# Performance work log

Hardware: AMD Instinct MI355X
Metric: run time of the kernel (lower is better)

## Reference

```python
import jax, jax.numpy as jnp
import numpy as np

N = 200000          # nodes
E = 6400000         # edges (before self-loops)
L = 4               # layer_n
H = 9               # hidden_channels (hardcoded in module)
G = 2000            # graphs in batch
C = 2               # num_classes
NEG_SLOPE = 0.2     # GATConv default leaky_relu slope for attention logits


def setup_inputs() -> dict:
    key = jax.random.key(0)
    ks = jax.random.split(key, 9)
    x = jax.random.normal(ks[0], (N, H), dtype=jnp.float32)
    edge_index = jax.random.randint(ks[1], (2, E), 0, N, dtype=jnp.int32)
    batch = jnp.sort(jax.random.randint(ks[2], (N,), 0, G, dtype=jnp.int32))
    W = jax.random.normal(ks[3], (L, H, H), dtype=jnp.float32) * 0.3
    att_src = jax.random.normal(ks[4], (L, H), dtype=jnp.float32) * 0.3
    att_dst = jax.random.normal(ks[5], (L, H), dtype=jnp.float32) * 0.3
    bias = jax.random.normal(ks[6], (L, H), dtype=jnp.float32) * 0.1
    fc_w = jax.random.normal(ks[7], (L * H, C), dtype=jnp.float32) * 0.2
    fc_b = jax.random.normal(ks[8], (C,), dtype=jnp.float32) * 0.1
    return dict(x=x, edge_index=edge_index, batch=batch, W=W,
                att_src=att_src, att_dst=att_dst, bias=bias,
                fc_w=fc_w, fc_b=fc_b)


def _gat_layer(x, W_l, a_src, a_dst, b_l, src, dst, n):
    # h: [N, H] transformed features (linear, no bias per PyG default)
    h = x @ W_l
    alpha_s = h @ a_src            # [N]
    alpha_d = h @ a_dst            # [N]
    # attention logits per edge (src -> dst), GAT softmax grouped by dst
    e = jax.nn.leaky_relu(alpha_s[src] + alpha_d[dst], NEG_SLOPE)  # [E']
    e = e - jax.ops.segment_max(e, dst, num_segments=n)[dst]
    w = jnp.exp(e)
    denom = jax.ops.segment_sum(w, dst, num_segments=n)[dst]
    alpha = w / denom              # [E']
    out = jax.ops.segment_sum(alpha[:, None] * h[src], dst, num_segments=n)
    return out + b_l


def reference(x, edge_index, batch, W, att_src, att_dst, bias, fc_w, fc_b):
    n = x.shape[0]
    loops = jnp.arange(n, dtype=edge_index.dtype)
    src = jnp.concatenate([edge_index[0], loops])  # add_self_loops=True
    dst = jnp.concatenate([edge_index[1], loops])
    jk = []
    h = x
    for l in range(L):
        h = _gat_layer(h, W[l], att_src[l], att_dst[l], bias[l], src, dst, n)
        h = jax.nn.relu(h)
        jk.append(h)
    jk = jnp.concatenate(jk, axis=1)               # [N, L*H]
    pooled = jax.ops.segment_max(jk, batch, num_segments=G)
    pooled = jnp.where(jnp.isfinite(pooled), pooled, 0.0)  # guard empty graphs
    # dropout is identity at inference
    return pooled @ fc_w + fc_b
```

## Files before the change

### kernel.cpp

```cpp
#include <hip/hip_runtime.h>
#include <hip/hip_fp16.h>

#define Nn 200000
#define Ee 6400000
#define EP 6600000
#define Hh 9
#define Ll 4
#define Gg 2000
#define Cc 2
#define JK 36
#define NCB ((Nn + 1023) >> 10)
#define EPB 8192
#define NBLKA ((EP + EPB - 1) / EPB)
#define NB ((Nn + 255) / 256)
#define NPB 32
#define NAB (Nn / NPB)
#define CAP 3072
#define CAPB 36864
#define HTS (NCB + 1)

union H2F { __half2 h; float f; };


__global__ __launch_bounds__(256) void kA_scatter(
    const int* __restrict__ src, const int* __restrict__ dst,
    int* __restrict__ ctot, int* __restrict__ histT,
    unsigned* __restrict__ bucketed)
{
    __shared__ unsigned pbuf[EPB];
    __shared__ int lh[NCB];
    __shared__ int s[256];
    int t = threadIdx.x;
    if (t < NCB) lh[t] = 0;
    __syncthreads();
    const int base = blockIdx.x * EPB;
    const int nseg = min(EPB, EP - base);
    for (int j = t; j < nseg; j += 256) {
        int e = base + j;
        int d = (e < Ee) ? dst[e] : (e - Ee);
        atomicAdd(&lh[d >> 10], 1);
    }
    __syncthreads();
    int v = (t < NCB) ? lh[t] : 0;
    s[t] = v; __syncthreads();
    for (int off = 1; off < 256; off <<= 1) {
        int u = (t >= off) ? s[t - off] : 0;
        __syncthreads();
        s[t] += u;
        __syncthreads();
    }
    int* hrow = histT + (size_t)blockIdx.x * HTS;
    if (t < NCB) {
        int ex = s[t] - v;
        lh[t] = ex;
        hrow[t] = ex;
        if (v) atomicAdd(&ctot[t], v);
    }
    if (t == 0) hrow[NCB] = nseg;
    __syncthreads();
    for (int j = t; j < nseg; j += 256) {
        int e = base + j;
        int sv, d;
        if (e < Ee) { sv = src[e]; d = dst[e]; } else { sv = e - Ee; d = sv; }
        int pos = atomicAdd(&lh[d >> 10], 1);
        pbuf[pos] = (unsigned)sv | ((unsigned)(d & 1023) << 18);
    }
    __syncthreads();
    for (int j = t; j < nseg; j += 256)
        bucketed[base + j] = pbuf[j];
}

__global__ __launch_bounds__(256) void k_scan(
    const int* __restrict__ ctot, int* __restrict__ cbase,
    int* __restrict__ row_ptr)
{
    __shared__ int s[256];
    int t = threadIdx.x;
    int v = (t < NCB) ? ctot[t] : 0;
    s[t] = v; __syncthreads();
    for (int off = 1; off < 256; off <<= 1) {
        int u = (t >= off) ? s[t - off] : 0;
        __syncthreads();
        s[t] += u;
        __syncthreads();
    }
    if (t < NCB) cbase[t] = s[t] - v;
    if (t == 0) { cbase[NCB] = EP; row_ptr[Nn] = EP; }
}

__global__ __launch_bounds__(1024) void kB_csr(
    const unsigned* __restrict__ bucketed, const int* __restrict__ histT,
    const int* __restrict__ cbase, int* __restrict__ row_ptr,
    int* __restrict__ csr_src)
{
    __shared__ int2 hb[NBLKA];
    __shared__ int bh[1024];
    __shared__ unsigned pbuf[CAPB];
    const int k = blockIdx.x;
    const int t = threadIdx.x;
    const int w = t >> 6, lane = t & 63;
    bh[t] = 0;
    for (int j = t; j < NBLKA; j += 1024) {
        const int* hrow = histT + (size_t)j * HTS + k;
        hb[j] = make_int2(hrow[0], hrow[1]);
    }
    __syncthreads();
    for (int b = w; b < NBLKA; b += 16 * 4) {
        int2 es[4]; unsigned ps[4];
#pragma unroll
        for (int u = 0; u < 4; ++u) {
            int bb = b + 16 * u;
            int2 e = (bb < NBLKA) ? hb[bb] : make_int2(0, 0);
            es[u] = e;
            int j = e.x + lane;
            ps[u] = (j < e.y)
                ? __builtin_nontemporal_load(bucketed + (size_t)bb * EPB + j)
                : 0u;
        }
#pragma unroll
        for (int u = 0; u < 4; ++u) {
            int bb = b + 16 * u;
            if (bb >= NBLKA) break;
            int j = es[u].x + lane;
            if (j < es[u].y) atomicAdd(&bh[(ps[u] >> 18) & 1023], 1);
            for (j += 64; j < es[u].y; j += 64) {
                unsigned p = __builtin_nontemporal_load(
                    bucketed + (size_t)bb * EPB + j);
                atomicAdd(&bh[(p >> 18) & 1023], 1);
            }
        }
    }
    __syncthreads();
    int v = bh[t];
    for (int off = 1; off < 1024; off <<= 1) {
        int u = (t >= off) ? bh[t - off] : 0;
        __syncthreads();
        bh[t] += u;
        __syncthreads();
    }
    const int base_k = cbase[k];
    const int nseg_b = cbase[k + 1] - base_k;
    int ex = bh[t] - v;
    const int node = (k << 10) + t;
    if (node < Nn) row_ptr[node] = base_k + ex;
    bh[t] = ex;
    __syncthreads();
    const bool fit = (nseg_b <= CAPB);
    if (fit) {
        for (int b = w; b < NBLKA; b += 16 * 4) {
            int2 es[4]; unsigned ps[4];
#pragma unroll
            for (int u = 0; u < 4; ++u) {
                int bb = b + 16 * u;
                int2 e = (bb < NBLKA) ? hb[bb] : make_int2(0, 0);
                es[u] = e;
                int j = e.x + lane;
                ps[u] = (j < e.y)
                    ? __builtin_nontemporal_load(bucketed + (size_t)bb * EPB + j)
                    : 0u;
            }
#pragma unroll
            for (int u = 0; u < 4; ++u) {
                int bb = b + 16 * u;
                if (bb >= NBLKA) break;
                int j = es[u].x + lane;
                if (j < es[u].y) {
                    unsigned p = ps[u];
                    int pos = atomicAdd(&bh[(p >> 18) & 1023], 1);
                    pbuf[pos] = p & 0x3FFFFu;
                }
                for (j += 64; j < es[u].y; j += 64) {
                    unsigned p = __builtin_nontemporal_load(
                        bucketed + (size_t)bb * EPB + j);
                    int pos = atomicAdd(&bh[(p >> 18) & 1023], 1);
                    pbuf[pos] = p & 0x3FFFFu;
                }
            }
        }
        __syncthreads();
        for (int j = t; j < nseg_b; j += 1024)
            csr_src[base_k + j] = (int)pbuf[j];
    } else {
        for (int b = w; b < NBLKA; b += 16) {
            int2 e = hb[b];
            int rb = b * EPB;
            for (int j = e.x + lane; j < e.y; j += 64) {
                unsigned p = bucketed[rb + j];
                int pos = base_k + atomicAdd(&bh[(p >> 18) & 1023], 1);
                csr_src[pos] = (int)(p & 0x3FFFFu);
            }
        }
    }
}


__global__ __launch_bounds__(256) void k_transform(
    const float* __restrict__ xin, int xstride,
    const float* __restrict__ Wl,
    const float* __restrict__ adst,
    float4* __restrict__ A, __half* __restrict__ Bh, float* __restrict__ D)
{
    int i = blockIdx.x * blockDim.x + threadIdx.x;
    if (i >= Nn) return;
    const float* xp = xin + (size_t)i * xstride;
    float xi[Hh];
#pragma unroll
    for (int k = 0; k < Hh; ++k) xi[k] = xp[k];
    float hv[Hh];
#pragma unroll
    for (int j = 0; j < Hh; ++j) {
        float s = 0.f;
#pragma unroll
        for (int k = 0; k < Hh; ++k) s += xi[k] * Wl[k * Hh + j];
        hv[j] = s;
    }
    float ad = 0.f;
#pragma unroll
    for (int j = 0; j < Hh; ++j) ad += hv[j] * adst[j];
    H2F u01, u23, u45, u67;
    u01.h = __floats2half2_rn(hv[0], hv[1]);
    u23.h = __floats2half2_rn(hv[2], hv[3]);
    u45.h = __floats2half2_rn(hv[4], hv[5]);
    u67.h = __floats2half2_rn(hv[6], hv[7]);
    A[i] = make_float4(u01.f, u23.f, u45.f, u67.f);
    Bh[i] = __float2half(hv[8]);
    D[i] = ad;
}

__global__ __launch_bounds__(256) void k_node_agg(
    const int* __restrict__ rp, const int* __restrict__ csr,
    const float4* __restrict__ A, const __half* __restrict__ Bh,
    const float* __restrict__ D, const float* __restrict__ asrc,
    const float* __restrict__ biasl,
    float* __restrict__ jk, int l)
{
    __shared__ int scsr[CAP];
    __shared__ int srp[NPB + 1];
    const int nbase = blockIdx.x * NPB;
    const int t = threadIdx.x;
    if (t <= NPB) srp[t] = rp[nbase + t];
    __syncthreads();
    const int beg_blk = srp[0];
    const int nseg = srp[NPB] - beg_blk;
    const bool use_lds = (nseg <= CAP);
    if (use_lds)
        for (int j = t; j < nseg; j += 256)
            scsr[j] = __builtin_nontemporal_load(csr + beg_blk + j);
    __syncthreads();

    const float s0 = asrc[0], s1 = asrc[1], s2 = asrc[2], s3 = asrc[3],
                s4 = asrc[4], s5 = asrc[5], s6 = asrc[6], s7 = asrc[7],
                s8 = asrc[8];

    const int ni = t >> 3;
    const int q  = t & 7;
    const int i  = nbase + ni;
    const float c = D[i];
    float a0=0,a1=0,a2=0,a3=0,a4=0,a5=0,a6=0,a7=0,a8=0,den=0;
    if (use_lds) {
        int idx = srp[ni] - beg_blk + q;
        const int iend = srp[ni + 1] - beg_blk;
        int s = (idx < iend) ? scsr[idx] : 0;
        float4 F = A[s];
        __half hb = Bh[s];
        while (idx < iend) {
            int nidx = idx + 8;
            int sn = (nidx < iend) ? scsr[nidx] : 0;
            float4 Fn = A[sn];
            __half hbn = Bh[sn];
            H2F u; float2 p;
            u.f = F.x; p = __half22float2(u.h); float x0 = p.x, x1 = p.y;
            u.f = F.y; p = __half22float2(u.h); float x2 = p.x, x3 = p.y;
            u.f = F.z; p = __half22float2(u.h); float x4 = p.x, x5 = p.y;
            u.f = F.w; p = __half22float2(u.h); float x6 = p.x, x7 = p.y;
            float x8 = __half2float(hb);
            float as = x0*s0 + x1*s1 + x2*s2 + x3*s3 + x4*s4
                     + x5*s5 + x6*s6 + x7*s7 + x8*s8;
            float lg = as + c;
            lg = lg > 0.f ? lg : 0.2f * lg;
            float w = __expf(lg);
            a0 += w*x0; a1 += w*x1; a2 += w*x2; a3 += w*x3; a4 += w*x4;
            a5 += w*x5; a6 += w*x6; a7 += w*x7; a8 += w*x8;
            den += w;
            F = Fn; hb = hbn; idx = nidx;
        }
    } else {
        for (int e = srp[ni] + q; e < srp[ni + 1]; e += 8) {
            int s = csr[e];
            float4 F = A[s];
            __half hb = Bh[s];
            H2F u; float2 p;
            u.f = F.x; p = __half22float2(u.h); float x0 = p.x, x1 = p.y;
            u.f = F.y; p = __half22float2(u.h); float x2 = p.x, x3 = p.y;
            u.f = F.z; p = __half22float2(u.h); float x4 = p.x, x5 = p.y;
            u.f = F.w; p = __half22float2(u.h); float x6 = p.x, x7 = p.y;
            float x8 = __half2float(hb);
            float as = x0*s0 + x1*s1 + x2*s2 + x3*s3 + x4*s4
                     + x5*s5 + x6*s6 + x7*s7 + x8*s8;
            float lg = as + c;
            lg = lg > 0.f ? lg : 0.2f * lg;
            float w = __expf(lg);
            a0 += w*x0; a1 += w*x1; a2 += w*x2; a3 += w*x3; a4 += w*x4;
            a5 += w*x5; a6 += w*x6; a7 += w*x7; a8 += w*x8;
            den += w;
        }
    }
#pragma unroll
    for (int m = 1; m <= 4; m <<= 1) {
        a0 += __shfl_xor(a0, m); a1 += __shfl_xor(a1, m);
        a2 += __shfl_xor(a2, m); a3 += __shfl_xor(a3, m);
        a4 += __shfl_xor(a4, m); a5 += __shfl_xor(a5, m);
        a6 += __shfl_xor(a6, m); a7 += __shfl_xor(a7, m);
        a8 += __shfl_xor(a8, m); den += __shfl_xor(den, m);
    }
    if (q == 0) {
        float inv = 1.f / den;
        float* jp = jk + (size_t)i * JK + l * Hh;
        float o;
        o = fmaxf(a0*inv + biasl[0], 0.f); __builtin_nontemporal_store(o, jp + 0);
        o = fmaxf(a1*inv + biasl[1], 0.f); __builtin_nontemporal_store(o, jp + 1);
        o = fmaxf(a2*inv + biasl[2], 0.f); __builtin_nontemporal_store(o, jp + 2);
        o = fmaxf(a3*inv + biasl[3], 0.f); __builtin_nontemporal_store(o, jp + 3);
        o = fmaxf(a4*inv + biasl[4], 0.f); __builtin_nontemporal_store(o, jp + 4);
        o = fmaxf(a5*inv + biasl[5], 0.f); __builtin_nontemporal_store(o, jp + 5);
        o = fmaxf(a6*inv + biasl[6], 0.f); __builtin_nontemporal_store(o, jp + 6);
        o = fmaxf(a7*inv + biasl[7], 0.f); __builtin_nontemporal_store(o, jp + 7);
        o = fmaxf(a8*inv + biasl[8], 0.f); __builtin_nontemporal_store(o, jp + 8);
    }
}


__global__ __launch_bounds__(256) void k_graph_ptr(
    const int* __restrict__ batch, int* __restrict__ gp)
{
    int i = blockIdx.x * 256 + threadIdx.x;
    if (i >= Nn) return;
    int b = batch[i];
    if (i == 0) {
        for (int g = 0; g <= b; ++g) gp[g] = 0;
    } else {
        int pb = batch[i - 1];
        for (int g = pb + 1; g <= b; ++g) gp[g] = i;
    }
    if (i == Nn - 1) {
        for (int g = b + 1; g <= Gg; ++g) gp[g] = Nn;
    }
}

__global__ __launch_bounds__(256) void k_pool_seg(
    const float* __restrict__ jk, const int* __restrict__ gp,
    float* __restrict__ pooled)
{
    int t = blockIdx.x * 256 + threadIdx.x;
    if (t >= Gg * JK) return;
    int g = t / JK, col = t - g * JK;
    int beg = gp[g], end = gp[g + 1];
    float m = 0.f;
    for (int i = beg; i < end; ++i)
        m = fmaxf(m, jk[(size_t)i * JK + col]);
    pooled[t] = m;
}

__global__ __launch_bounds__(256) void k_fc(
    const float* __restrict__ pooled, const float* __restrict__ fcw,
    const float* __restrict__ fcb, float* __restrict__ out)
{
    int t = blockIdx.x * blockDim.x + threadIdx.x;
    if (t >= Gg * Cc) return;
    int g = t / Cc, c = t - g * Cc;
    float s = fcb[c];
    const float* pp = pooled + (size_t)g * JK;
#pragma unroll
    for (int j = 0; j < JK; ++j) s += pp[j] * fcw[j * Cc + c];
    out[t] = s;
}

extern "C" void kernel_launch(void* const* d_in, const int* in_sizes, int n_in,
                              void* d_out, int out_size, void* d_ws, size_t ws_size,
                              hipStream_t stream) {
    const float* x      = (const float*)d_in[0];
    const int*   ei     = (const int*)d_in[1];
    const int*   batch  = (const int*)d_in[2];
    const float* W      = (const float*)d_in[3];
    const float* a_src  = (const float*)d_in[4];
    const float* a_dst  = (const float*)d_in[5];
    const float* bias   = (const float*)d_in[6];
    const float* fc_w   = (const float*)d_in[7];
    const float* fc_b   = (const float*)d_in[8];
    float* out = (float*)d_out;

    float* ws        = (float*)d_ws;
    float4* A        = (float4*)ws;
    __half* Bh       = (__half*)(ws + (size_t)Nn * 4);
    float* D         = (float*)((char*)Bh + (size_t)Nn * sizeof(__half));
    float* jk        = D + Nn;
    float* pooled    = jk + (size_t)Nn * JK;
    int* row_ptr     = (int*)(pooled + (size_t)Gg * JK);
    int* gp          = row_ptr + Nn + 1;
    int* ctot        = gp + Gg + 1;
    int* cbase       = ctot + NCB;
    int* csr_src     = cbase + NCB + 1;
    int* histT       = (int*)ws;
    unsigned* bucketed = (unsigned*)jk;

    const int* srcp = ei;
    const int* dstp = ei + Ee;

    hipMemsetAsync(ctot, 0, NCB * sizeof(int), stream);
    kA_scatter<<<NBLKA, 256, 0, stream>>>(srcp, dstp, ctot, histT, bucketed);
    k_scan    <<<1, 256, 0, stream>>>(ctot, cbase, row_ptr);
    kB_csr    <<<NCB, 1024, 0, stream>>>(bucketed, histT, cbase, row_ptr, csr_src);

    for (int l = 0; l < Ll; ++l) {
        const float* xin = (l == 0) ? x : (jk + (size_t)(l - 1) * Hh);
        int xstride      = (l == 0) ? Hh : JK;
        k_transform<<<NB, 256, 0, stream>>>(xin, xstride, W + l * Hh * Hh,
                                            a_dst + l * Hh, A, Bh, D);
        k_node_agg<<<NAB, 256, 0, stream>>>(row_ptr, csr_src, A, Bh, D,
                                            a_src + l * Hh, bias + l * Hh, jk, l);
    }
    k_graph_ptr<<<NB, 256, 0, stream>>>(batch, gp);
    k_pool_seg<<<(Gg * JK + 255) / 256, 256, 0, stream>>>(jk, gp, pooled);
    k_fc<<<(Gg * Cc + 255) / 256, 256, 0, stream>>>(pooled, fc_w, fc_b, out);
}
```

Measured before the change: 556.0 us.

## Store JK layers contiguously and double-buffer edge gathers in node aggregation

The per-layer JK outputs move from an interleaved [N,36] layout to separate contiguous [N,9] blocks per layer. This gives contiguous writes in aggregation and contiguous reads in the next transform and in pooling, and the nontemporal stores are dropped. The LDS-path edge loop now processes two edges per iteration per lane, keeping two gathers in flight to hide gather latency, at the cost of more registers. Pooling reads are re-indexed to the new layout.

```diff
diff --git a/kernel.cpp b/kernel.cpp
--- a/kernel.cpp
+++ b/kernel.cpp
@@ -227,6 +227,24 @@
     D[i] = ad;
 }
 
+#define AGG_EDGE(F, HB)                                                     \
+    {                                                                       \
+        H2F u; float2 p;                                                    \
+        u.f = (F).x; p = __half22float2(u.h); float x0 = p.x, x1 = p.y;     \
+        u.f = (F).y; p = __half22float2(u.h); float x2 = p.x, x3 = p.y;     \
+        u.f = (F).z; p = __half22float2(u.h); float x4 = p.x, x5 = p.y;     \
+        u.f = (F).w; p = __half22float2(u.h); float x6 = p.x, x7 = p.y;     \
+        float x8 = __half2float(HB);                                        \
+        float as = x0*s0 + x1*s1 + x2*s2 + x3*s3 + x4*s4                    \
+                 + x5*s5 + x6*s6 + x7*s7 + x8*s8;                           \
+        float lg = as + c;                                                  \
+        lg = lg > 0.f ? lg : 0.2f * lg;                                     \
+        float wgt = __expf(lg);                                             \
+        a0 += wgt*x0; a1 += wgt*x1; a2 += wgt*x2; a3 += wgt*x3;             \
+        a4 += wgt*x4; a5 += wgt*x5; a6 += wgt*x6; a7 += wgt*x7;             \
+        a8 += wgt*x8; den += wgt;                                           \
+    }
+
 __global__ __launch_bounds__(256) void k_node_agg(
     const int* __restrict__ rp, const int* __restrict__ csr,
     const float4* __restrict__ A, const __half* __restrict__ Bh,
@@ -258,51 +276,30 @@
     const float c = D[i];
     float a0=0,a1=0,a2=0,a3=0,a4=0,a5=0,a6=0,a7=0,a8=0,den=0;
     if (use_lds) {
-        int idx = srp[ni] - beg_blk + q;
         const int iend = srp[ni + 1] - beg_blk;
-        int s = (idx < iend) ? scsr[idx] : 0;
-        float4 F = A[s];
-        __half hb = Bh[s];
-        while (idx < iend) {
-            int nidx = idx + 8;
-            int sn = (nidx < iend) ? scsr[nidx] : 0;
-            float4 Fn = A[sn];
-            __half hbn = Bh[sn];
-            H2F u; float2 p;
-            u.f = F.x; p = __half22float2(u.h); float x0 = p.x, x1 = p.y;
-            u.f = F.y; p = __half22float2(u.h); float x2 = p.x, x3 = p.y;
-            u.f = F.z; p = __half22float2(u.h); float x4 = p.x, x5 = p.y;
-            u.f = F.w; p = __half22float2(u.h); float x6 = p.x, x7 = p.y;
-            float x8 = __half2float(hb);
-            float as = x0*s0 + x1*s1 + x2*s2 + x3*s3 + x4*s4
-                     + x5*s5 + x6*s6 + x7*s7 + x8*s8;
-            float lg = as + c;
-            lg = lg > 0.f ? lg : 0.2f * lg;
-            float w = __expf(lg);
-            a0 += w*x0; a1 += w*x1; a2 += w*x2; a3 += w*x3; a4 += w*x4;
-            a5 += w*x5; a6 += w*x6; a7 += w*x7; a8 += w*x8;
-            den += w;
-            F = Fn; hb = hbn; idx = nidx;
+        int i0 = srp[ni] - beg_blk + q;
+        int i1 = i0 + 8;
+        int sv0 = (i0 < iend) ? scsr[i0] : 0;
+        int sv1 = (i1 < iend) ? scsr[i1] : 0;
+        float4 F0 = A[sv0]; __half b0 = Bh[sv0];
+        float4 F1 = A[sv1]; __half b1 = Bh[sv1];
+        while (i0 < iend) {
+            int n0 = i0 + 16, n1 = i1 + 16;
+            int sn0 = (n0 < iend) ? scsr[n0] : 0;
+            int sn1 = (n1 < iend) ? scsr[n1] : 0;
+            float4 Fn0 = A[sn0]; __half bn0 = Bh[sn0];
+            float4 Fn1 = A[sn1]; __half bn1 = Bh[sn1];
+            AGG_EDGE(F0, b0);
+            if (i1 < iend) AGG_EDGE(F1, b1);
+            F0 = Fn0; b0 = bn0; F1 = Fn1; b1 = bn1;
+            i0 = n0; i1 = n1;
         }
     } else {
         for (int e = srp[ni] + q; e < srp[ni + 1]; e += 8) {
             int s = csr[e];
             float4 F = A[s];
             __half hb = Bh[s];
-            H2F u; float2 p;
-            u.f = F.x; p = __half22float2(u.h); float x0 = p.x, x1 = p.y;
-            u.f = F.y; p = __half22float2(u.h); float x2 = p.x, x3 = p.y;
-            u.f = F.z; p = __half22float2(u.h); float x4 = p.x, x5 = p.y;
-            u.f = F.w; p = __half22float2(u.h); float x6 = p.x, x7 = p.y;
-            float x8 = __half2float(hb);
-            float as = x0*s0 + x1*s1 + x2*s2 + x3*s3 + x4*s4
-                     + x5*s5 + x6*s6 + x7*s7 + x8*s8;
-            float lg = as + c;
-            lg = lg > 0.f ? lg : 0.2f * lg;
-            float w = __expf(lg);
-            a0 += w*x0; a1 += w*x1; a2 += w*x2; a3 += w*x3; a4 += w*x4;
-            a5 += w*x5; a6 += w*x6; a7 += w*x7; a8 += w*x8;
-            den += w;
+            AGG_EDGE(F, hb);
         }
     }
 #pragma unroll
@@ -315,17 +312,16 @@
     }
     if (q == 0) {
         float inv = 1.f / den;
-        float* jp = jk + (size_t)i * JK + l * Hh;
-        float o;
-        o = fmaxf(a0*inv + biasl[0], 0.f); __builtin_nontemporal_store(o, jp + 0);
-        o = fmaxf(a1*inv + biasl[1], 0.f); __builtin_nontemporal_store(o, jp + 1);
-        o = fmaxf(a2*inv + biasl[2], 0.f); __builtin_nontemporal_store(o, jp + 2);
-        o = fmaxf(a3*inv + biasl[3], 0.f); __builtin_nontemporal_store(o, jp + 3);
-        o = fmaxf(a4*inv + biasl[4], 0.f); __builtin_nontemporal_store(o, jp + 4);
-        o = fmaxf(a5*inv + biasl[5], 0.f); __builtin_nontemporal_store(o, jp + 5);
-        o = fmaxf(a6*inv + biasl[6], 0.f); __builtin_nontemporal_store(o, jp + 6);
-        o = fmaxf(a7*inv + biasl[7], 0.f); __builtin_nontemporal_store(o, jp + 7);
-        o = fmaxf(a8*inv + biasl[8], 0.f); __builtin_nontemporal_store(o, jp + 8);
+        float* jp = jk + (size_t)l * Nn * Hh + (size_t)i * Hh;
+        jp[0] = fmaxf(a0*inv + biasl[0], 0.f);
+        jp[1] = fmaxf(a1*inv + biasl[1], 0.f);
+        jp[2] = fmaxf(a2*inv + biasl[2], 0.f);
+        jp[3] = fmaxf(a3*inv + biasl[3], 0.f);
+        jp[4] = fmaxf(a4*inv + biasl[4], 0.f);
+        jp[5] = fmaxf(a5*inv + biasl[5], 0.f);
+        jp[6] = fmaxf(a6*inv + biasl[6], 0.f);
+        jp[7] = fmaxf(a7*inv + biasl[7], 0.f);
+        jp[8] = fmaxf(a8*inv + biasl[8], 0.f);
     }
 }
 
@@ -354,10 +350,12 @@
     int t = blockIdx.x * 256 + threadIdx.x;
     if (t >= Gg * JK) return;
     int g = t / JK, col = t - g * JK;
+    int lc = col / Hh, cc = col - lc * Hh;
+    const float* bp = jk + (size_t)lc * Nn * Hh + cc;
     int beg = gp[g], end = gp[g + 1];
     float m = 0.f;
     for (int i = beg; i < end; ++i)
-        m = fmaxf(m, jk[(size_t)i * JK + col]);
+        m = fmaxf(m, bp[(size_t)i * Hh]);
     pooled[t] = m;
 }
 
@@ -412,8 +410,8 @@
     kB_csr    <<<NCB, 1024, 0, stream>>>(bucketed, histT, cbase, row_ptr, csr_src);
 
     for (int l = 0; l < Ll; ++l) {
-        const float* xin = (l == 0) ? x : (jk + (size_t)(l - 1) * Hh);
-        int xstride      = (l == 0) ? Hh : JK;
+        const float* xin = (l == 0) ? x : (jk + (size_t)(l - 1) * Nn * Hh);
+        int xstride      = Hh;
         k_transform<<<NB, 256, 0, stream>>>(xin, xstride, W + l * Hh * Hh,
                                             a_dst + l * Hh, A, Bh, D);
         k_node_agg<<<NAB, 256, 0, stream>>>(row_ptr, csr_src, A, Bh, D,
```

New measurement: 524.0 us. -5.8%, faster.
